# Optimization experiments

Measured on AMD Instinct MI355X. Metric: run time of the kernel, lower is better.

The kernel has to match this reference:

```python
import jax, jax.numpy as jnp
import numpy as np

N_QUBITS = 6
N_QLAYERS = 3
LOGISTIC_R = 3.99
HENON_A, HENON_B = 1.4, 0.3


def _conv1d(x, w, b):
    # x: [B, C_in, T], w: [C_out, C_in, K=3], SAME padding (pad=1)
    y = jax.lax.conv_general_dilated(x, w, window_strides=(1,), padding=((1, 1),),
                                     dimension_numbers=('NCH', 'OIH', 'NCH'))
    return y + b[None, :, None]


def _apply_1q_batched(state, G, q):
    # state: [B,2,...,2], G: [B,2,2] acting on qubit axis 1+q
    s = jnp.moveaxis(state, 1 + q, -1)
    s = jnp.einsum('bij,b...j->b...i', G, s)
    return jnp.moveaxis(s, -1, 1 + q)


def _apply_1q(state, G, q):
    s = jnp.moveaxis(state, 1 + q, -1)
    s = jnp.einsum('ij,b...j->b...i', G, s)
    return jnp.moveaxis(s, -1, 1 + q)


def _apply_cnot(state, c, t):
    s = jnp.moveaxis(state, (1 + c, 1 + t), (-2, -1))
    # control=1 block: flip target amplitudes
    s = jnp.concatenate([s[..., 0:1, :], s[..., 1:2, ::-1]], axis=-2)
    return jnp.moveaxis(s, (-2, -1), (1 + c, 1 + t))


def quantum_expvals(angles, qweights):
    # angles: [B, 6] real encoding angles; qweights: [3, 6] shared RY params
    B = angles.shape[0]
    state = jnp.zeros((B, 2 ** N_QUBITS), jnp.complex64).at[:, 0].set(1.0)
    state = state.reshape((B,) + (2,) * N_QUBITS)
    half = 0.5 * angles
    for i in range(N_QUBITS):
        ax = half[:, i % N_QUBITS]
        ay = half[:, (i + 1) % N_QUBITS]
        az = half[:, (i + 2) % N_QUBITS]
        cx_, sx_ = jnp.cos(ax), jnp.sin(ax)
        RX = jnp.stack([jnp.stack([cx_ + 0j, -1j * sx_], -1),
                        jnp.stack([-1j * sx_, cx_ + 0j], -1)], -2)
        state = _apply_1q_batched(state, RX, i)
        cy_, sy_ = jnp.cos(ay), jnp.sin(ay)
        RY = jnp.stack([jnp.stack([cy_ + 0j, -sy_ + 0j], -1),
                        jnp.stack([sy_ + 0j, cy_ + 0j], -1)], -2)
        state = _apply_1q_batched(state, RY, i)
        ez = jnp.exp(1j * az)
        zero = jnp.zeros_like(ez)
        RZ = jnp.stack([jnp.stack([jnp.conj(ez), zero], -1),
                        jnp.stack([zero, ez], -1)], -2)
        state = _apply_1q_batched(state, RZ, i)
    for l in range(N_QLAYERS):
        for q in range(N_QUBITS):
            a = 0.5 * qweights[l, q]
            c_, s_ = jnp.cos(a), jnp.sin(a)
            RY = jnp.array([[1., 0.], [0., 1.]], jnp.float32) * c_ + \
                 jnp.array([[0., -1.], [1., 0.]], jnp.float32) * s_
            state = _apply_1q(state, RY.astype(jnp.complex64), q)
        for q in range(N_QUBITS):
            state = _apply_cnot(state, q, (q + 1) % N_QUBITS)
    probs = (state * jnp.conj(state)).real  # [B,2,...,2]
    evs = []
    for i in range(N_QUBITS):
        axes = tuple(a for a in range(1, N_QUBITS + 1) if a != 1 + i)
        p = jnp.sum(probs, axis=axes)  # [B,2]
        evs.append(p[:, 0] - p[:, 1])
    return jnp.stack(evs, -1)  # [B,6]


def _lstm_cell(xt, h, c, Wih, Whh, bih, bhh):
    g = xt @ Wih.T + bih + h @ Whh.T + bhh
    i, f, gg, o = jnp.split(g, 4, axis=-1)
    c2 = jax.nn.sigmoid(f) * c + jax.nn.sigmoid(i) * jnp.tanh(gg)
    h2 = jax.nn.sigmoid(o) * jnp.tanh(c2)
    return h2, c2


def _forward(x, w0, b0, w1, b1, w2, b2, Wih, Whh, bih, bhh, qweights, Wfc, bfc, Wout, bout):
    B = x.shape[0]
    t = x.transpose(0, 2, 1)                 # [B, C, T]
    t = jax.nn.relu(_conv1d(t, w0, b0))
    t = jax.nn.relu(_conv1d(t, w1, b1))
    t = jax.nn.relu(_conv1d(t, w2, b2))
    t = t.transpose(2, 0, 1)                 # [T, B, H]
    H = t.shape[2]
    h0 = jnp.zeros((B, H), x.dtype)
    c0 = jnp.zeros((B, H), x.dtype)

    def step(carry, xt):
        h, c = carry
        h, c = _lstm_cell(xt, h, c, Wih, Whh, bih, bhh)
        h = LOGISTIC_R * h * (1.0 - h)
        x0, y0 = h[:, 0], h[:, 1]
        xn = 1.0 - HENON_A * x0 ** 2 + y0
        yn = HENON_B * x0
        h = jnp.concatenate([xn[:, None], yn[:, None], h[:, 2:]], axis=1)
        # QuantumRNNCell called as qrnn(hx, hx): h = h + fc(quantum(h[:, :6]))
        h = h + quantum_expvals(h[:, :N_QUBITS], qweights) @ Wfc.T + bfc
        return (h, c), None

    (h, _), _ = jax.lax.scan(step, (h0, c0), t)
    return jax.nn.sigmoid(h @ Wout.T + bout)  # [B, 1]


def setup_inputs() -> dict:
    key = jax.random.key(0)
    ks = jax.random.split(key, 20)
    B, T, D, Htcn, Hlstm = 1024, 256, 64, 32, 32
    s = 0.1
    inp = {
        'x': jax.random.normal(ks[0], (B, T, D), jnp.float32),
        'w0': jax.random.normal(ks[1], (Htcn, D, 3), jnp.float32) * s,
        'b0': jax.random.normal(ks[2], (Htcn,), jnp.float32) * s,
        'w1': jax.random.normal(ks[3], (Htcn, Htcn, 3), jnp.float32) * s,
        'b1': jax.random.normal(ks[4], (Htcn,), jnp.float32) * s,
        'w2': jax.random.normal(ks[5], (Htcn, Htcn, 3), jnp.float32) * s,
        'b2': jax.random.normal(ks[6], (Htcn,), jnp.float32) * s,
        'Wih': jax.random.normal(ks[7], (4 * Hlstm, Htcn), jnp.float32) * s,
        'Whh': jax.random.normal(ks[8], (4 * Hlstm, Hlstm), jnp.float32) * s,
        'bih': jax.random.normal(ks[9], (4 * Hlstm,), jnp.float32) * s,
        'bhh': jax.random.normal(ks[10], (4 * Hlstm,), jnp.float32) * s,
        'qweights': jax.random.normal(ks[11], (N_QLAYERS, N_QUBITS), jnp.float32),
        'Wfc': jax.random.normal(ks[12], (Hlstm, N_QUBITS), jnp.float32) * s,
        'bfc': jax.random.normal(ks[13], (Hlstm,), jnp.float32) * s,
        'Wout': jax.random.normal(ks[14], (1, Hlstm), jnp.float32) * s,
        'bout': jax.random.normal(ks[15], (1,), jnp.float32) * s,
    }
    return inp


def reference(x, w0, b0, w1, b1, w2, b2, Wih, Whh, bih, bhh, qweights, Wfc, bfc, Wout, bout):
    return _forward(x, w0, b0, w1, b1, w2, b2, Wih, Whh, bih, bhh, qweights, Wfc, bfc, Wout, bout)
```

## Files before the change

### kernel.cpp

```cpp
#include <hip/hip_runtime.h>

#define B_SIZE 1024
#define T_LEN  256
#define D_IN   64
#define HC     32

typedef int   v2i_t __attribute__((ext_vector_type(2)));
typedef float v2f   __attribute__((ext_vector_type(2)));

__device__ __forceinline__ float frcp(float x){ return __builtin_amdgcn_rcpf(x); }
__device__ __forceinline__ float rfl(float x){
    return __uint_as_float(__builtin_amdgcn_readfirstlane(__float_as_uint(x)));
}
__device__ __forceinline__ float rdlane(float x, int l){
    return __int_as_float(__builtin_amdgcn_readlane(__float_as_int(x), l));
}
__device__ __forceinline__ float ftanh(float x){
    return 1.f - 2.f*frcp(__expf(2.f*x) + 1.f);
}
__device__ __forceinline__ float fsigmoid(float x){
    return frcp(1.f + __expf(-x));
}

template<int CTRL>
__device__ __forceinline__ int dppmov(int x){
    return __builtin_amdgcn_update_dpp(x, x, CTRL, 0xF, 0xF, false);
}

template<int M>
__device__ __forceinline__ int dpp_xor(int x){
    static_assert(M >= 1 && M <= 15, "dpp_xor mask");
    constexpr int hi = M & 12;
    constexpr int q  = (hi == 4 || hi == 12) ? ((M & 3) ^ 3) : (M & 3);
    if constexpr (q == 1) x = dppmov<0xB1>(x);
    else if constexpr (q == 2) x = dppmov<0x4E>(x);
    else if constexpr (q == 3) x = dppmov<0x1B>(x);
    if constexpr (hi == 4)       x = dppmov<0x141>(x);
    else if constexpr (hi == 8)  x = dppmov<0x128>(x);
    else if constexpr (hi == 12) x = dppmov<0x140>(x);
    return x;
}

#if defined(__has_builtin)
#  if __has_builtin(__builtin_amdgcn_permlane16_swap)
#    define HAVE_PL16 1
#  endif
#endif

template<int M>
__device__ __forceinline__ float xshuf(float xf){
    if constexpr (M == 0) return xf;
    int x = __float_as_int(xf);
    if constexpr (M & 15) x = dpp_xor<M & 15>(x);
    if constexpr (M & 16){
#ifdef HAVE_PL16
        v2i_t r = __builtin_amdgcn_permlane16_swap(x, x, false, false);
        x = r.x ^ r.y ^ x;
#else
        x = __builtin_amdgcn_ds_swizzle(x, (16 << 10) | 0x1F);
#endif
    }
    if constexpr (M & 32){
        v2i_t r = __builtin_amdgcn_permlane32_swap(x, x, false, false);
        x = r.x ^ r.y ^ x;
    }
    return __int_as_float(x);
}

struct QMasks { int M[3][6]; int S[3][6]; int R[6]; };
constexpr QMasks qmasks(){
    QMasks qm{};
    unsigned m[6], n[6];
    for (int i = 0; i < 6; i++){ m[i] = 1u << i; n[i] = 1u << i; }
    for (int l = 0; l < 3; l++){
        for (int q = 0; q < 6; q++){
            unsigned u = m[q], r = 0;
            for (int i = 0; i < 6; i++) if ((u >> i) & 1u) r |= (32u >> i);
            qm.S[l][q] = (int)r;
            unsigned u2 = 0;
            for (int i = 0; i < 6; i++) u2 |= ((n[i] >> q) & 1u) << i;
            unsigned r2 = 0;
            for (int i = 0; i < 6; i++) if ((u2 >> i) & 1u) r2 |= (32u >> i);
            qm.M[l][q] = (int)r2;
        }
        for (int q = 0; q < 6; q++) m[(q + 1) % 6] ^= m[q];
        n[0] ^= n[5];
        for (int q = 4; q >= 0; q--) n[q + 1] ^= n[q];
    }
    for (int i = 0; i < 6; i++){
        unsigned u = m[i], r = 0;
        for (int j = 0; j < 6; j++) if ((u >> j) & 1u) r |= (32u >> j);
        qm.R[i] = (int)r;
    }
    return qm;
}
constexpr QMasks QM = qmasks();

__global__ __launch_bounds__(256) void conv0_kernel(const float* __restrict__ x,
    const float* __restrict__ w0, const float* __restrict__ b0, float* __restrict__ out)
{
    __shared__ float xs[130*65];
    __shared__ float wl[192*32];
    const int tid = threadIdx.x;
    const int b  = blockIdx.x >> 1;
    const int s0 = (blockIdx.x & 1) * 128;

    for (int idx = tid; idx < 130*64; idx += 256){
        int r = idx >> 6, d = idx & 63;
        int s = s0 - 1 + r;
        float v = 0.f;
        if (s >= 0 && s < T_LEN) v = x[(size_t)b*(T_LEN*D_IN) + (size_t)s*D_IN + d];
        xs[r*65 + d] = v;
    }
    for (int idx = tid; idx < 192*32; idx += 256){
        int r = idx >> 5, c = idx & 31;
        wl[idx] = w0[c*192 + r];
    }
    __syncthreads();

    const int c0 = (tid & 7) * 4;
    const int sl = (tid >> 3) * 4;
    float acc[4][4];
    #pragma unroll
    for (int ci = 0; ci < 4; ci++){
        float bb = b0[c0+ci];
        #pragma unroll
        for (int m = 0; m < 4; m++) acc[ci][m] = bb;
    }
    for (int d = 0; d < 64; d++){
        float xv[6];
        #pragma unroll
        for (int o = 0; o < 6; o++) xv[o] = xs[(sl+o)*65 + d];
        #pragma unroll
        for (int kk = 0; kk < 3; kk++){
            const float4 wv = *(const float4*)&wl[(d*3+kk)*32 + c0];
            float w4[4] = {wv.x, wv.y, wv.z, wv.w};
            #pragma unroll
            for (int ci = 0; ci < 4; ci++)
                #pragma unroll
                for (int m = 0; m < 4; m++)
                    acc[ci][m] += xv[m+kk]*w4[ci];
        }
    }
    #pragma unroll
    for (int ci = 0; ci < 4; ci++){
        float4 v;
        v.x = fmaxf(acc[ci][0], 0.f); v.y = fmaxf(acc[ci][1], 0.f);
        v.z = fmaxf(acc[ci][2], 0.f); v.w = fmaxf(acc[ci][3], 0.f);
        *(float4*)&out[(size_t)b*(HC*T_LEN) + (size_t)(c0+ci)*T_LEN + (s0+sl)] = v;
    }
}

template<bool TOUT>
__global__ __launch_bounds__(256) void convm_kernel(const float* __restrict__ in,
    const float* __restrict__ w, const float* __restrict__ bias, float* __restrict__ out)
{
    __shared__ float xs[130*33];
    __shared__ float wl[96*32];
    const int tid = threadIdx.x;
    const int b  = blockIdx.x >> 1;
    const int s0 = (blockIdx.x & 1) * 128;

    for (int idx = tid; idx < 32*130; idx += 256){
        int ci = idx / 130; int r = idx - ci*130;
        int s = s0 - 1 + r;
        float v = 0.f;
        if (s >= 0 && s < T_LEN) v = in[(size_t)b*(HC*T_LEN) + (size_t)ci*T_LEN + s];
        xs[r*33 + ci] = v;
    }
    for (int idx = tid; idx < 96*32; idx += 256){
        int r = idx >> 5, c = idx & 31;
        wl[idx] = w[c*96 + r];
    }
    __syncthreads();

    const int c0 = (tid & 7) * 4;
    const int sl = (tid >> 3) * 4;
    float acc[4][4];
    #pragma unroll
    for (int ci = 0; ci < 4; ci++){
        float bb = bias[c0+ci];
        #pragma unroll
        for (int m = 0; m < 4; m++) acc[ci][m] = bb;
    }
    for (int ci2 = 0; ci2 < 32; ci2++){
        float xv[6];
        #pragma unroll
        for (int o = 0; o < 6; o++) xv[o] = xs[(sl+o)*33 + ci2];
        #pragma unroll
        for (int kk = 0; kk < 3; kk++){
            const float4 wv = *(const float4*)&wl[(ci2*3+kk)*32 + c0];
            float w4[4] = {wv.x, wv.y, wv.z, wv.w};
            #pragma unroll
            for (int ci = 0; ci < 4; ci++)
                #pragma unroll
                for (int m = 0; m < 4; m++)
                    acc[ci][m] += xv[m+kk]*w4[ci];
        }
    }
    if (!TOUT){
        #pragma unroll
        for (int ci = 0; ci < 4; ci++){
            float4 v;
            v.x = fmaxf(acc[ci][0], 0.f); v.y = fmaxf(acc[ci][1], 0.f);
            v.z = fmaxf(acc[ci][2], 0.f); v.w = fmaxf(acc[ci][3], 0.f);
            *(float4*)&out[(size_t)b*(HC*T_LEN) + (size_t)(c0+ci)*T_LEN + (s0+sl)] = v;
        }
    } else {
        #pragma unroll
        for (int m = 0; m < 4; m++){
            int s = s0 + sl + m;
            float4 v;
            v.x = fmaxf(acc[0][m], 0.f); v.y = fmaxf(acc[1][m], 0.f);
            v.z = fmaxf(acc[2][m], 0.f); v.w = fmaxf(acc[3][m], 0.f);
            *(float4*)&out[(size_t)s*(B_SIZE*HC) + (size_t)b*HC + c0] = v;
        }
    }
}

__global__ __launch_bounds__(256) void gates_kernel(const float* __restrict__ tS,
    const float* __restrict__ Wih, const float* __restrict__ bih,
    const float* __restrict__ bhh, float* __restrict__ G)
{
    __shared__ float xs[8][32];
    const int tid = threadIdx.x;
    const size_t pair0 = (size_t)blockIdx.x * 8;

    { int p = tid >> 5, j = tid & 31;
      xs[p][j] = tS[pair0*32 + (size_t)p*32 + j]; }
    __syncthreads();

    const int r = tid & 127;
    const int half = tid >> 7;
    float4 wr[8];
    #pragma unroll
    for (int j4 = 0; j4 < 8; j4++) wr[j4] = ((const float4*)Wih)[r*8 + j4];
    const float br = bih[r] + bhh[r];

    #pragma unroll
    for (int pp = 0; pp < 4; pp++){
        const int p = half + pp*2;
        float a0 = br, a1 = 0.f, a2 = 0.f, a3 = 0.f;
        #pragma unroll
        for (int j4 = 0; j4 < 8; j4++){
            const float4 xv = *(const float4*)&xs[p][j4*4];
            a0 += wr[j4].x*xv.x; a1 += wr[j4].y*xv.y;
            a2 += wr[j4].z*xv.z; a3 += wr[j4].w*xv.w;
        }
        G[(pair0 + p)*128 + r] = (a0+a1)+(a2+a3);
    }
}

__global__ __launch_bounds__(256, 1) void scan_kernel(
    const float* __restrict__ G,   const float* __restrict__ Whh,
    const float* __restrict__ qw,  const float* __restrict__ Wfc,
    const float* __restrict__ bfc, const float* __restrict__ Wout,
    const float* __restrict__ bout, float* __restrict__ out)
{
    const unsigned lane = threadIdx.x & 63u;
    const int wv   = threadIdx.x >> 6;
    const int b    = __builtin_amdgcn_readfirstlane(blockIdx.x * 4 + wv);
    const int r1 = lane, r2 = lane + 64;
    const int k  = lane & 31;

    v2f uAB[32];
    #pragma unroll
    for (int j4 = 0; j4 < 8; j4++){
        float4 d_ = ((const float4*)Whh)[r1*8 + j4];
        float4 e  = ((const float4*)Whh)[r2*8 + j4];
        uAB[j4*4+0] = v2f{d_.x, e.x}; uAB[j4*4+1] = v2f{d_.y, e.y};
        uAB[j4*4+2] = v2f{d_.z, e.z}; uAB[j4*4+3] = v2f{d_.w, e.w};
    }

    float wfcr[6];
    #pragma unroll
    for (int j = 0; j < 6; j++) wfcr[j] = Wfc[k*6 + j];
    const float bfcl  = bfc[k];
    const float woutl = (lane < 32) ? Wout[k] : 0.f;
    const float boutv = bout[0];

    float cgv[18], ssin[18];
    #pragma unroll
    for (int g = 0; g < 18; g++){
        int l = g / 6, q = g % 6;
        float a = 0.5f * qw[g];
        float cv = __cosf(a), sv = __sinf(a);
        cgv[g] = rfl(cv);
        unsigned sm = (unsigned)QM.S[l][q];
        ssin[g] = (__builtin_popcount(sm & lane) & 1) ? sv : -sv;
    }
    float wsgn[6];
    #pragma unroll
    for (int j = 0; j < 6; j++) wsgn[j] = (lane & (1u << j)) ? -1.f : 1.f;
    const bool qs[6] = { (lane & 32u) != 0, (lane & 16u) != 0, (lane & 8u) != 0,
                         (lane & 4u) != 0,  (lane & 2u) != 0,  (lane & 1u) != 0 };

    float h = 0.f, c = 0.f;
    const float* gbase = G + (size_t)b*128;
    float g1 = gbase[r1], g2 = gbase[r2];

    #pragma clang loop unroll(disable)
    for (int s = 0; s < T_LEN; s++){
        const float cg1 = g1, cg2 = g2;
        {
            int s2 = (s + 1 < T_LEN) ? s + 1 : s;
            const float* gn = gbase + (size_t)s2*(B_SIZE*128);
            g1 = gn[r1]; g2 = gn[r2];
        }

        v2f a0 = v2f{cg1, cg2}, a1 = v2f{0.f,0.f}, a2 = v2f{0.f,0.f}, a3 = v2f{0.f,0.f};
        #pragma unroll
        for (int j = 0; j < 32; j += 4){
            float h0 = rdlane(h, j),   h1 = rdlane(h, j+1);
            float h2 = rdlane(h, j+2), h3 = rdlane(h, j+3);
            a0 += h0*uAB[j]; a1 += h1*uAB[j+1]; a2 += h2*uAB[j+2]; a3 += h3*uAB[j+3];
        }
        v2f accv = (a0+a1)+(a2+a3);
        float acc1 = accv.x, acc2 = accv.y;

        float sigA = fsigmoid(acc1);
        float argB = (lane < 32) ? acc2 : 0.5f*acc2;
        float tt   = ftanh(argB);
        float actB = (lane < 32) ? tt : (0.5f + 0.5f*tt);
        float fsig = xshuf<32>(sigA);
        float osig = xshuf<32>(actB);
        c = fsig*c + sigA*actB;
        float hn = osig * ftanh(c);

        hn = 3.99f * hn * (1.f - hn);
        float x0 = rdlane(hn, 0), y0 = rdlane(hn, 1);
        float xnv = 1.f - 1.4f*x0*x0 + y0;
        float ynv = 0.3f * x0;

        float ang[6];
        ang[0] = 0.5f*xnv; ang[1] = 0.5f*ynv;
        ang[2] = 0.5f*rdlane(hn, 2); ang[3] = 0.5f*rdlane(hn, 3);
        ang[4] = 0.5f*rdlane(hn, 4); ang[5] = 0.5f*rdlane(hn, 5);
        float ca[6], sa[6];
        #pragma unroll
        for (int j = 0; j < 6; j++){ ca[j] = __cosf(ang[j]); sa[j] = __sinf(ang[j]); }

        float fr[6], fi[6];
        #pragma unroll
        for (int i = 0; i < 6; i++){
            const int i1 = (i+1)%6, i2 = (i+2)%6;
            float cx=ca[i], sx=sa[i], cy=ca[i1], sy=sa[i1], cz=ca[i2], sz=sa[i2];
            float w0r = cy*cx, w0i = sy*sx;
            float w1r = sy*cx, w1i = -cy*sx;
            float q0r = cz*w0r + sz*w0i, q0i = cz*w0i - sz*w0r;
            float q1r = cz*w1r - sz*w1i, q1i = cz*w1i + sz*w1r;
            fr[i] = qs[i] ? q1r : q0r;
            fi[i] = qs[i] ? q1i : q0i;
        }
        v2f t01 = v2f{fr[0]*fr[1] - fi[0]*fi[1], fr[0]*fi[1] + fi[0]*fr[1]};
        v2f t23 = v2f{fr[2]*fr[3] - fi[2]*fi[3], fr[2]*fi[3] + fi[2]*fr[3]};
        v2f t45 = v2f{fr[4]*fr[5] - fi[4]*fi[5], fr[4]*fi[5] + fi[4]*fr[5]};
        v2f t03 = v2f{t01.x*t23.x - t01.y*t23.y, t01.x*t23.y + t01.y*t23.x};
        v2f av  = v2f{t03.x*t45.x - t03.y*t45.y, t03.x*t45.y + t03.y*t45.x};

        #define GATE(L,Q) { \
            constexpr int MM = QM.M[L][Q]; \
            v2f bv; bv.x = xshuf<MM>(av.x); bv.y = xshuf<MM>(av.y); \
            av = cgv[(L)*6+(Q)]*av + ssin[(L)*6+(Q)]*bv; }
        GATE(0,0) GATE(0,1) GATE(0,2) GATE(0,3) GATE(0,4) GATE(0,5)
        GATE(1,0) GATE(1,1) GATE(1,2) GATE(1,3) GATE(1,4) GATE(1,5)
        GATE(2,0) GATE(2,1) GATE(2,2) GATE(2,3) GATE(2,4) GATE(2,5)
        #undef GATE

        float wp = av.x*av.x + av.y*av.y;
        wp = wsgn[0]*wp + xshuf< 1>(wp);
        wp = wsgn[1]*wp + xshuf< 2>(wp);
        wp = wsgn[2]*wp + xshuf< 4>(wp);
        wp = wsgn[3]*wp + xshuf< 8>(wp);
        wp = wsgn[4]*wp + xshuf<16>(wp);
        wp = wsgn[5]*wp + xshuf<32>(wp);
        float ev0 = rdlane(wp, QM.R[0]), ev1 = rdlane(wp, QM.R[1]);
        float ev2 = rdlane(wp, QM.R[2]), ev3 = rdlane(wp, QM.R[3]);
        float ev4 = rdlane(wp, QM.R[4]), ev5 = rdlane(wp, QM.R[5]);

        float upd = bfcl + (wfcr[0]*ev0 + wfcr[1]*ev1)
                         + (wfcr[2]*ev2 + wfcr[3]*ev3)
                         + (wfcr[4]*ev4 + wfcr[5]*ev5);

        float hsel = hn;
        hsel = (lane == 0u) ? xnv : hsel;
        hsel = (lane == 1u) ? ynv : hsel;
        h = hsel + upd;
    }

    float pv = (lane < 32) ? h*woutl : 0.f;
    #pragma unroll
    for (int off = 32; off; off >>= 1) pv += __shfl_xor(pv, off, 64);
    if (lane == 0) out[b] = fsigmoid(pv + boutv);
}

__global__ __launch_bounds__(256, 1) void scan_legacy(
    const float* __restrict__ tS,
    const float* __restrict__ Wih, const float* __restrict__ Whh,
    const float* __restrict__ bih, const float* __restrict__ bhh,
    const float* __restrict__ qw,  const float* __restrict__ Wfc,
    const float* __restrict__ bfc, const float* __restrict__ Wout,
    const float* __restrict__ bout, float* __restrict__ out)
{
    const unsigned lane = threadIdx.x & 63u;
    const int wv   = threadIdx.x >> 6;
    const int b    = __builtin_amdgcn_readfirstlane(blockIdx.x * 4 + wv);
    const int r1 = lane, r2 = lane + 64;
    const int k  = lane & 31;

    float wA[32], wB[32], uA[32], uB[32];
    #pragma unroll
    for (int j4 = 0; j4 < 8; j4++){
        float4 a  = ((const float4*)Wih)[r1*8 + j4];
        float4 c_ = ((const float4*)Wih)[r2*8 + j4];
        float4 d_ = ((const float4*)Whh)[r1*8 + j4];
        float4 e  = ((const float4*)Whh)[r2*8 + j4];
        wA[j4*4+0]=a.x;  wA[j4*4+1]=a.y;  wA[j4*4+2]=a.z;  wA[j4*4+3]=a.w;
        wB[j4*4+0]=c_.x; wB[j4*4+1]=c_.y; wB[j4*4+2]=c_.z; wB[j4*4+3]=c_.w;
        uA[j4*4+0]=d_.x; uA[j4*4+1]=d_.y; uA[j4*4+2]=d_.z; uA[j4*4+3]=d_.w;
        uB[j4*4+0]=e.x;  uB[j4*4+1]=e.y;  uB[j4*4+2]=e.z;  uB[j4*4+3]=e.w;
    }
    const float bias1 = bih[r1] + bhh[r1];
    const float bias2 = bih[r2] + bhh[r2];

    float wfcr[6];
    #pragma unroll
    for (int j = 0; j < 6; j++) wfcr[j] = Wfc[k*6 + j];
    const float bfcl  = bfc[k];
    const float woutl = (lane < 32) ? Wout[k] : 0.f;
    const float boutv = bout[0];

    float cgv[18], ssin[18];
    #pragma unroll
    for (int g = 0; g < 18; g++){
        int l = g / 6, q = g % 6;
        float a = 0.5f * qw[g];
        float cv = __cosf(a), sv = __sinf(a);
        cgv[g] = rfl(cv);
        unsigned sm = (unsigned)QM.S[l][q];
        ssin[g] = (__builtin_popcount(sm & lane) & 1) ? sv : -sv;
    }
    float wsgn[6];
    #pragma unroll
    for (int j = 0; j < 6; j++) wsgn[j] = (lane & (1u << j)) ? -1.f : 1.f;
    const bool qs[6] = { (lane & 32u) != 0, (lane & 16u) != 0, (lane & 8u) != 0,
                         (lane & 4u) != 0,  (lane & 2u) != 0,  (lane & 1u) != 0 };

    float h = 0.f, c = 0.f;
    const float* xbase = tS + (size_t)b * HC;

    float4 xf[8];
    #pragma unroll
    for (int j4 = 0; j4 < 8; j4++) xf[j4] = ((const float4*)xbase)[j4];

    #pragma clang loop unroll(disable)
    for (int s = 0; s < T_LEN; s++){
        float xt[32];
        #pragma unroll
        for (int j4 = 0; j4 < 8; j4++){
            xt[j4*4+0]=xf[j4].x; xt[j4*4+1]=xf[j4].y; xt[j4*4+2]=xf[j4].z; xt[j4*4+3]=xf[j4].w;
        }
        {
            int s2 = (s + 1 < T_LEN) ? s + 1 : s;
            const float4* np_ = (const float4*)(xbase + (size_t)s2*(B_SIZE*HC));
            #pragma unroll
            for (int j4 = 0; j4 < 8; j4++) xf[j4] = np_[j4];
        }

        float a1a = bias1, a1b = 0.f, a2a = bias2, a2b = 0.f;
        #pragma unroll
        for (int j = 0; j < 32; j += 2){
            a1a += xt[j]*wA[j];     a1b += xt[j+1]*wA[j+1];
            a2a += xt[j]*wB[j];     a2b += xt[j+1]*wB[j+1];
        }
        #pragma unroll
        for (int j = 0; j < 32; j += 2){
            float h0 = rdlane(h, j), h1 = rdlane(h, j+1);
            a1a += h0*uA[j];   a1b += h1*uA[j+1];
            a2a += h0*uB[j];   a2b += h1*uB[j+1];
        }
        float acc1 = a1a + a1b, acc2 = a2a + a2b;

        float sigA = fsigmoid(acc1);
        float argB = (lane < 32) ? acc2 : 0.5f*acc2;
        float tt   = ftanh(argB);
        float actB = (lane < 32) ? tt : (0.5f + 0.5f*tt);
        float fsig = xshuf<32>(sigA);
        float osig = xshuf<32>(actB);
        c = fsig*c + sigA*actB;
        float hn = osig * ftanh(c);

        hn = 3.99f * hn * (1.f - hn);
        float x0 = rdlane(hn, 0), y0 = rdlane(hn, 1);
        float xnv = 1.f - 1.4f*x0*x0 + y0;
        float ynv = 0.3f * x0;

        float ang[6];
        ang[0] = 0.5f*xnv; ang[1] = 0.5f*ynv;
        ang[2] = 0.5f*rdlane(hn, 2); ang[3] = 0.5f*rdlane(hn, 3);
        ang[4] = 0.5f*rdlane(hn, 4); ang[5] = 0.5f*rdlane(hn, 5);
        float ca[6], sa[6];
        #pragma unroll
        for (int j = 0; j < 6; j++){ ca[j] = __cosf(ang[j]); sa[j] = __sinf(ang[j]); }

        float fr[6], fi[6];
        #pragma unroll
        for (int i = 0; i < 6; i++){
            const int i1 = (i+1)%6, i2 = (i+2)%6;
            float cx=ca[i], sx=sa[i], cy=ca[i1], sy=sa[i1], cz=ca[i2], sz=sa[i2];
            float w0r = cy*cx, w0i = sy*sx;
            float w1r = sy*cx, w1i = -cy*sx;
            float q0r = cz*w0r + sz*w0i, q0i = cz*w0i - sz*w0r;
            float q1r = cz*w1r - sz*w1i, q1i = cz*w1i + sz*w1r;
            fr[i] = qs[i] ? q1r : q0r;
            fi[i] = qs[i] ? q1i : q0i;
        }
        float t01r = fr[0]*fr[1] - fi[0]*fi[1], t01i = fr[0]*fi[1] + fi[0]*fr[1];
        float t23r = fr[2]*fr[3] - fi[2]*fi[3], t23i = fr[2]*fi[3] + fi[2]*fr[3];
        float t45r = fr[4]*fr[5] - fi[4]*fi[5], t45i = fr[4]*fi[5] + fi[4]*fr[5];
        float t03r = t01r*t23r - t01i*t23i,     t03i = t01r*t23i + t01i*t23r;
        float ar   = t03r*t45r - t03i*t45i,     ai   = t03r*t45i + t03i*t45r;

        #define GATE(L,Q) { \
            constexpr int MM = QM.M[L][Q]; \
            float br = xshuf<MM>(ar), bi = xshuf<MM>(ai); \
            float cg = cgv[(L)*6+(Q)], ss = ssin[(L)*6+(Q)]; \
            ar = cg*ar + ss*br; ai = cg*ai + ss*bi; }
        GATE(0,0) GATE(0,1) GATE(0,2) GATE(0,3) GATE(0,4) GATE(0,5)
        GATE(1,0) GATE(1,1) GATE(1,2) GATE(1,3) GATE(1,4) GATE(1,5)
        GATE(2,0) GATE(2,1) GATE(2,2) GATE(2,3) GATE(2,4) GATE(2,5)
        #undef GATE

        float wp = ar*ar + ai*ai;
        wp = wsgn[0]*wp + xshuf< 1>(wp);
        wp = wsgn[1]*wp + xshuf< 2>(wp);
        wp = wsgn[2]*wp + xshuf< 4>(wp);
        wp = wsgn[3]*wp + xshuf< 8>(wp);
        wp = wsgn[4]*wp + xshuf<16>(wp);
        wp = wsgn[5]*wp + xshuf<32>(wp);
        float ev0 = rdlane(wp, QM.R[0]), ev1 = rdlane(wp, QM.R[1]);
        float ev2 = rdlane(wp, QM.R[2]), ev3 = rdlane(wp, QM.R[3]);
        float ev4 = rdlane(wp, QM.R[4]), ev5 = rdlane(wp, QM.R[5]);

        float upd = bfcl + (wfcr[0]*ev0 + wfcr[1]*ev1)
                         + (wfcr[2]*ev2 + wfcr[3]*ev3)
                         + (wfcr[4]*ev4 + wfcr[5]*ev5);

        float hsel = hn;
        hsel = (lane == 0u) ? xnv : hsel;
        hsel = (lane == 1u) ? ynv : hsel;
        h = hsel + upd;
    }

    float pv = (lane < 32) ? h*woutl : 0.f;
    #pragma unroll
    for (int off = 32; off; off >>= 1) pv += __shfl_xor(pv, off, 64);
    if (lane == 0) out[b] = fsigmoid(pv + boutv);
}

extern "C" void kernel_launch(void* const* d_in, const int* in_sizes, int n_in,
                              void* d_out, int out_size, void* d_ws, size_t ws_size,
                              hipStream_t stream)
{
    (void)in_sizes; (void)n_in; (void)out_size;
    const float* x    = (const float*)d_in[0];
    const float* w0   = (const float*)d_in[1];
    const float* b0   = (const float*)d_in[2];
    const float* w1   = (const float*)d_in[3];
    const float* b1   = (const float*)d_in[4];
    const float* w2   = (const float*)d_in[5];
    const float* b2   = (const float*)d_in[6];
    const float* Wih  = (const float*)d_in[7];
    const float* Whh  = (const float*)d_in[8];
    const float* bih  = (const float*)d_in[9];
    const float* bhh  = (const float*)d_in[10];
    const float* qw   = (const float*)d_in[11];
    const float* Wfc  = (const float*)d_in[12];
    const float* bfc  = (const float*)d_in[13];
    const float* Wout = (const float*)d_in[14];
    const float* bout = (const float*)d_in[15];
    float* out = (float*)d_out;

    const size_t tensorN = (size_t)B_SIZE*HC*T_LEN;
    float* t0 = (float*)d_ws;
    float* t1 = t0 + tensorN;
    float* tS = t0;
    float* G  = t1 + tensorN;
    const size_t need = (2*tensorN + (size_t)T_LEN*B_SIZE*128) * sizeof(float);

    conv0_kernel<<<2048, 256, 0, stream>>>(x, w0, b0, t0);
    convm_kernel<false><<<2048, 256, 0, stream>>>(t0, w1, b1, t1);
    convm_kernel<true ><<<2048, 256, 0, stream>>>(t1, w2, b2, tS);
    if (ws_size >= need){
        gates_kernel<<<(T_LEN*B_SIZE)/8, 256, 0, stream>>>(tS, Wih, bih, bhh, G);
        scan_kernel<<<256, 256, 0, stream>>>(G, Whh, qw, Wfc, bfc, Wout, bout, out);
    } else {
        scan_legacy<<<256, 256, 0, stream>>>(tS, Wih, Whh, bih, bhh, qw, Wfc, bfc, Wout, bout, out);
    }
}
```

Baseline: 747.6 us.

## Fuse final conv layer with LSTM input-gate projection and pad weight tiles

The third conv layer and the input-gate projection now run in one kernel. The conv output tile stays in shared memory (reusing the input buffer after a barrier) and feeds the Wih projection directly, so the intermediate tensor no longer makes a global round trip and one launch is dropped. Weight staging in all conv kernels now reads global memory coalesced and writes a padded (stride 36) LDS layout. The cost is that each block now loops over 128 timesteps for gates instead of 8, so there are fewer, longer blocks with a larger shared-memory footprint.

```diff
diff --git a/kernel.cpp b/kernel.cpp
--- a/kernel.cpp
+++ b/kernel.cpp
@@ -99,8 +99,8 @@
 __global__ __launch_bounds__(256) void conv0_kernel(const float* __restrict__ x,
     const float* __restrict__ w0, const float* __restrict__ b0, float* __restrict__ out)
 {
-    __shared__ float xs[130*65];
-    __shared__ float wl[192*32];
+    __shared__ __align__(16) float xs[130*65];
+    __shared__ __align__(16) float wl[192*36];
     const int tid = threadIdx.x;
     const int b  = blockIdx.x >> 1;
     const int s0 = (blockIdx.x & 1) * 128;
@@ -113,8 +113,8 @@
         xs[r*65 + d] = v;
     }
     for (int idx = tid; idx < 192*32; idx += 256){
-        int r = idx >> 5, c = idx & 31;
-        wl[idx] = w0[c*192 + r];
+        int c = idx / 192, r = idx - c*192;
+        wl[r*36 + c] = w0[idx];
     }
     __syncthreads();
 
@@ -133,7 +133,7 @@
         for (int o = 0; o < 6; o++) xv[o] = xs[(sl+o)*65 + d];
         #pragma unroll
         for (int kk = 0; kk < 3; kk++){
-            const float4 wv = *(const float4*)&wl[(d*3+kk)*32 + c0];
+            const float4 wv = *(const float4*)&wl[(d*3+kk)*36 + c0];
             float w4[4] = {wv.x, wv.y, wv.z, wv.w};
             #pragma unroll
             for (int ci = 0; ci < 4; ci++)
@@ -155,8 +155,8 @@
 __global__ __launch_bounds__(256) void convm_kernel(const float* __restrict__ in,
     const float* __restrict__ w, const float* __restrict__ bias, float* __restrict__ out)
 {
-    __shared__ float xs[130*33];
-    __shared__ float wl[96*32];
+    __shared__ __align__(16) float xs[130*33];
+    __shared__ __align__(16) float wl[96*36];
     const int tid = threadIdx.x;
     const int b  = blockIdx.x >> 1;
     const int s0 = (blockIdx.x & 1) * 128;
@@ -169,8 +169,8 @@
         xs[r*33 + ci] = v;
     }
     for (int idx = tid; idx < 96*32; idx += 256){
-        int r = idx >> 5, c = idx & 31;
-        wl[idx] = w[c*96 + r];
+        int c = idx / 96, r = idx - c*96;
+        wl[r*36 + c] = w[idx];
     }
     __syncthreads();
 
@@ -189,7 +189,7 @@
         for (int o = 0; o < 6; o++) xv[o] = xs[(sl+o)*33 + ci2];
         #pragma unroll
         for (int kk = 0; kk < 3; kk++){
-            const float4 wv = *(const float4*)&wl[(ci2*3+kk)*32 + c0];
+            const float4 wv = *(const float4*)&wl[(ci2*3+kk)*36 + c0];
             float w4[4] = {wv.x, wv.y, wv.z, wv.w};
             #pragma unroll
             for (int ci = 0; ci < 4; ci++)
@@ -218,16 +218,65 @@
     }
 }
 
-__global__ __launch_bounds__(256) void gates_kernel(const float* __restrict__ tS,
+__global__ __launch_bounds__(256) void convm_gates_kernel(const float* __restrict__ in,
+    const float* __restrict__ w, const float* __restrict__ bias,
     const float* __restrict__ Wih, const float* __restrict__ bih,
     const float* __restrict__ bhh, float* __restrict__ G)
 {
-    __shared__ float xs[8][32];
+    __shared__ __align__(16) float smem[4292 + 3456];
+    float* xs = smem;
+    float* wl = smem + 4292;
+    float* ts = smem;
     const int tid = threadIdx.x;
-    const size_t pair0 = (size_t)blockIdx.x * 8;
-
-    { int p = tid >> 5, j = tid & 31;
-      xs[p][j] = tS[pair0*32 + (size_t)p*32 + j]; }
+    const int b  = blockIdx.x >> 1;
+    const int s0 = (blockIdx.x & 1) * 128;
+
+    for (int idx = tid; idx < 32*130; idx += 256){
+        int ci = idx / 130; int r = idx - ci*130;
+        int s = s0 - 1 + r;
+        float v = 0.f;
+        if (s >= 0 && s < T_LEN) v = in[(size_t)b*(HC*T_LEN) + (size_t)ci*T_LEN + s];
+        xs[r*33 + ci] = v;
+    }
+    for (int idx = tid; idx < 96*32; idx += 256){
+        int c = idx / 96, r = idx - c*96;
+        wl[r*36 + c] = w[idx];
+    }
+    __syncthreads();
+
+    const int c0 = (tid & 7) * 4;
+    const int sl = (tid >> 3) * 4;
+    float acc[4][4];
+    #pragma unroll
+    for (int ci = 0; ci < 4; ci++){
+        float bb = bias[c0+ci];
+        #pragma unroll
+        for (int m = 0; m < 4; m++) acc[ci][m] = bb;
+    }
+    for (int ci2 = 0; ci2 < 32; ci2++){
+        float xv[6];
+        #pragma unroll
+        for (int o = 0; o < 6; o++) xv[o] = xs[(sl+o)*33 + ci2];
+        #pragma unroll
+        for (int kk = 0; kk < 3; kk++){
+            const float4 wv = *(const float4*)&wl[(ci2*3+kk)*36 + c0];
+            float w4[4] = {wv.x, wv.y, wv.z, wv.w};
+            #pragma unroll
+            for (int ci = 0; ci < 4; ci++)
+                #pragma unroll
+                for (int m = 0; m < 4; m++)
+                    acc[ci][m] += xv[m+kk]*w4[ci];
+        }
+    }
+    __syncthreads();
+
+    #pragma unroll
+    for (int m = 0; m < 4; m++){
+        float4 v;
+        v.x = fmaxf(acc[0][m], 0.f); v.y = fmaxf(acc[1][m], 0.f);
+        v.z = fmaxf(acc[2][m], 0.f); v.w = fmaxf(acc[3][m], 0.f);
+        *(float4*)&ts[(sl+m)*36 + c0] = v;
+    }
     __syncthreads();
 
     const int r = tid & 127;
@@ -237,17 +286,15 @@
     for (int j4 = 0; j4 < 8; j4++) wr[j4] = ((const float4*)Wih)[r*8 + j4];
     const float br = bih[r] + bhh[r];
 
-    #pragma unroll
-    for (int pp = 0; pp < 4; pp++){
-        const int p = half + pp*2;
+    for (int ss = half; ss < 128; ss += 2){
         float a0 = br, a1 = 0.f, a2 = 0.f, a3 = 0.f;
         #pragma unroll
         for (int j4 = 0; j4 < 8; j4++){
-            const float4 xv = *(const float4*)&xs[p][j4*4];
+            const float4 xv = *(const float4*)&ts[ss*36 + j4*4];
             a0 += wr[j4].x*xv.x; a1 += wr[j4].y*xv.y;
             a2 += wr[j4].z*xv.z; a3 += wr[j4].w*xv.w;
         }
-        G[(pair0 + p)*128 + r] = (a0+a1)+(a2+a3);
+        G[((size_t)(s0+ss)*B_SIZE + b)*128 + r] = (a0+a1)+(a2+a3);
     }
 }
 
@@ -584,17 +631,17 @@
     const size_t tensorN = (size_t)B_SIZE*HC*T_LEN;
     float* t0 = (float*)d_ws;
     float* t1 = t0 + tensorN;
-    float* tS = t0;
     float* G  = t1 + tensorN;
     const size_t need = (2*tensorN + (size_t)T_LEN*B_SIZE*128) * sizeof(float);
 
     conv0_kernel<<<2048, 256, 0, stream>>>(x, w0, b0, t0);
     convm_kernel<false><<<2048, 256, 0, stream>>>(t0, w1, b1, t1);
-    convm_kernel<true ><<<2048, 256, 0, stream>>>(t1, w2, b2, tS);
     if (ws_size >= need){
-        gates_kernel<<<(T_LEN*B_SIZE)/8, 256, 0, stream>>>(tS, Wih, bih, bhh, G);
+        convm_gates_kernel<<<2048, 256, 0, stream>>>(t1, w2, b2, Wih, bih, bhh, G);
         scan_kernel<<<256, 256, 0, stream>>>(G, Whh, qw, Wfc, bfc, Wout, bout, out);
     } else {
+        float* tS = t0;
+        convm_kernel<true ><<<2048, 256, 0, stream>>>(t1, w2, b2, tS);
         scan_legacy<<<256, 256, 0, stream>>>(tS, Wih, Whh, bih, bhh, qw, Wfc, bfc, Wout, bout, out);
     }
 }
```

Result: faster. 660.4 us (-11.7%).
